# Optimization experiments

Measured on AMD Instinct MI355X. Metric: run time of the kernel, lower is better.

## Reference

```python
import jax, jax.numpy as jnp
import numpy as np

B, L, H, C, A = 8, 4096, 512, 64, 512
NEG = -1000000000.0

def setup_inputs() -> dict:
    key = jax.random.key(0)
    ks = jax.random.split(key, 6)
    hidden_states = jax.random.normal(ks[0], (B, L, H), dtype=jnp.float32)
    critical_mask = jax.random.randint(ks[1], (B, L, 1), 0, 2).astype(bool)
    count_active_channels = jax.random.randint(ks[2], (B, L, 1), 0, 64).astype(jnp.int32)
    channel_activity = jax.random.normal(ks[3], (B, L, C), dtype=jnp.float32)
    proj_w = jax.random.normal(ks[4], (H, A), dtype=jnp.float32) * 0.02
    proj_b = jnp.zeros((A,), dtype=jnp.float32)
    score_w = jax.random.normal(ks[5], (A, 1), dtype=jnp.float32) * 0.02
    score_b = jnp.zeros((1,), dtype=jnp.float32)
    return {"hidden_states": hidden_states, "critical_mask": critical_mask,
            "count_active_channels": count_active_channels,
            "channel_activity": channel_activity,
            "proj_w": proj_w, "proj_b": proj_b,
            "score_w": score_w, "score_b": score_b}

def reference(hidden_states, critical_mask, count_active_channels, channel_activity,
              proj_w, proj_b, score_w, score_b):
    mask = critical_mask[..., 0].astype(bool)                       # (B,L)
    count_signal = count_active_channels[..., 0].astype(hidden_states.dtype)  # (B,L)
    activity = jnp.maximum(channel_activity.astype(hidden_states.dtype), 0.0)  # (B,L,C)
    # score(tanh(proj(h)))  -> (B,L)
    logits = (jnp.tanh(hidden_states @ proj_w + proj_b) @ score_w + score_b)[..., 0]
    logits = logits + jnp.log1p(jnp.maximum(count_signal, 0.0))
    channel_mask = activity > 0                                      # (B,L,C)
    # (B,C,L) masked logits with log1p activity bias
    channel_logits = logits[:, None, :] + jnp.log1p(jnp.swapaxes(activity, 1, 2))
    channel_logits = jnp.where(jnp.swapaxes(channel_mask, 1, 2), channel_logits, NEG)
    has_channel_any = channel_mask.any(axis=1)                       # (B,C)
    weights = jax.nn.softmax(channel_logits, axis=-1)                # (B,C,L)
    weights = jnp.where(has_channel_any[..., None], weights, 0.0)
    channel_contexts = jnp.einsum('bcl,blh->bch', weights, hidden_states)  # (B,C,H)
    fallback = jnp.broadcast_to(hidden_states[:, -1:, :], channel_contexts.shape)
    channel_contexts = jnp.where(has_channel_any[..., None], channel_contexts, fallback)
    mix = activity / jnp.maximum(activity.sum(axis=2, keepdims=True), 1.0)  # (B,L,C)
    expanded_context = jnp.einsum('blc,bch->blh', mix, channel_contexts)    # (B,L,H)
    max_count = jnp.maximum(count_signal.max(axis=1, keepdims=True), 1.0)
    density_gate = 1.0 + count_signal / max_count                    # (B,L)
    attended = jnp.where(mask[..., None], expanded_context * density_gate[..., None], hidden_states)
    return attended, weights
```

## Files before the change

### kernel.cpp

```cpp
#include <hip/hip_runtime.h>
#include <hip/hip_bf16.h>
#include <math.h>

#define NEGV (-1000000000.0f)
constexpr int Bb = 8, Ll = 4096, Hh = 512, Cc = 64, Aa = 512;

typedef float f32x4 __attribute__((ext_vector_type(4)));
typedef short s16x8 __attribute__((ext_vector_type(8)));

__device__ inline ushort f2bf(float f) {
  union { float f; uint u; } v; v.f = f;
  uint u = v.u;
  return (ushort)((u + 0x7FFFu + ((u >> 16) & 1u)) >> 16);
}

__device__ __forceinline__ void gl16(const void* g, void* l) {
  __builtin_amdgcn_global_load_lds(
      reinterpret_cast<const __attribute__((address_space(1))) unsigned int*>(
          reinterpret_cast<uintptr_t>(g)),
      reinterpret_cast<__attribute__((address_space(3))) unsigned int*>(
          reinterpret_cast<uintptr_t>(l)),
      16, 0, 0);
}

__global__ __launch_bounds__(256) void k_front(
    const float* __restrict__ hid, const int* __restrict__ cnt,
    const float* __restrict__ sb, const float* __restrict__ pw,
    ushort* __restrict__ hidb, ushort* __restrict__ hidbT,
    float* __restrict__ logits, ushort* __restrict__ pwT,
    int* __restrict__ cmax) {
  __shared__ ushort sh[64 * 66];
  const int bid = blockIdx.x;
  const int tid = threadIdx.x;

  if (bid < 4096) {
    const int b = bid >> 9;
    const int rem = bid & 511;
    const int h0 = (rem >> 6) * 64;
    const int l0 = (rem & 63) * 64;
    const int lr = tid >> 6;
    const int hc = tid & 63;
#pragma unroll
    for (int i = 0; i < 16; ++i) {
      int l = lr + i * 4;
      ushort v = f2bf(hid[((size_t)(b * Ll + l0 + l)) * Hh + h0 + hc]);
      sh[l * 65 + hc] = v;
      hidb[((size_t)(b * Ll + l0 + l)) * Hh + h0 + hc] = v;
    }
    __syncthreads();
#pragma unroll
    for (int i = 0; i < 8; ++i) {
      int e = tid + i * 256;
      int ht = e >> 5, p = e & 31;
      uint v = (uint)sh[(2 * p) * 65 + ht] | ((uint)sh[(2 * p + 1) * 65 + ht] << 16);
      *(uint*)(hidbT + ((size_t)(b * Hh + h0 + ht)) * Ll + l0 + 2 * p) = v;
    }
  } else if (bid < 4160) {
    const int bx = bid - 4096;
    const int k0 = (bx >> 3) * 64, a0 = (bx & 7) * 64;
#pragma unroll
    for (int i = 0; i < 16; ++i) {
      int e = tid + i * 256;
      int kk = e >> 6, aa = e & 63;
      sh[aa * 65 + kk] = f2bf(pw[(size_t)(k0 + kk) * Aa + a0 + aa]);
    }
    __syncthreads();
#pragma unroll
    for (int i = 0; i < 16; ++i) {
      int e = tid + i * 256;
      int aa = e >> 6, kk = e & 63;
      pwT[(size_t)(a0 + aa) * Hh + k0 + kk] = sh[aa * 65 + kk];
    }
  } else if (bid < 4288) {
    int i = (bid - 4160) * 256 + tid;
    logits[i] = sb[0] + log1pf(fmaxf((float)cnt[i], 0.f));
  } else {
    int* shi = (int*)sh;
    const int b = bid - 4288;
    const int* p = cnt + b * Ll;
    int m = 0;
#pragma unroll
    for (int j = 0; j < 16; ++j) m = max(m, p[tid + j * 256]);
#pragma unroll
    for (int s = 32; s; s >>= 1) m = max(m, __shfl_xor(m, s));
    if ((tid & 63) == 0) shi[tid >> 6] = m;
    __syncthreads();
    if (tid == 0)
      cmax[b] = max(max(shi[0], shi[1]), max(shi[2], shi[3]));
  }
}

__global__ __launch_bounds__(256) void k0_gemm(
    const ushort* __restrict__ hidb, const ushort* __restrict__ pwT,
    const float* __restrict__ pb, const float* __restrict__ sw,
    float* __restrict__ logits) {
  __shared__ ushort smem[16384];
  const int bm = blockIdx.x, bn = blockIdx.y;
  const int tid = threadIdx.x;
  const int lane = tid & 63;
  const int w = tid >> 6;
  const int wm = w >> 1, wn = w & 1;
  const int lc = lane & 15, lq = lane >> 4;

  const int srow = tid >> 2;
  const int schunk = (tid & 3) * 8;
  const ushort* Ag = hidb + ((size_t)(bm * 128 + srow)) * Hh + schunk;
  const ushort* Bg = pwT + ((size_t)(bn * 128 + srow)) * Hh + schunk;
  const int wrow = 16 * w;

  f32x4 acc[4][4];
#pragma unroll
  for (int mi = 0; mi < 4; ++mi)
#pragma unroll
    for (int ni = 0; ni < 4; ++ni) acc[mi][ni] = (f32x4){0.f, 0.f, 0.f, 0.f};

  const int aoffc = (wm * 64 + lc) * 32 + lq * 8;
  const int boffc = (wn * 64 + lc) * 32 + lq * 8;

#define K0_STAGE(buf, kb)                                   \
  do {                                                      \
    const ushort* ag = Ag + (kb) * 32;                      \
    const ushort* bg = Bg + (kb) * 32;                      \
    ushort* la = smem + (buf) * 4096 + wrow * 32;           \
    ushort* lb = smem + 8192 + (buf) * 4096 + wrow * 32;    \
    gl16(ag, la);                                           \
    gl16(ag + 64 * Hh, la + 64 * 32);                       \
    gl16(bg, lb);                                           \
    gl16(bg + 64 * Hh, lb + 64 * 32);                       \
  } while (0)

  K0_STAGE(0, 0);
  __syncthreads();

  int buf = 0;
  for (int kb = 0; kb < 16; ++kb) {
    if (kb < 15) K0_STAGE(buf ^ 1, kb + 1);
    const ushort* Ab = smem + buf * 4096;
    const ushort* Bt = smem + 8192 + buf * 4096;
    s16x8 af[4], bfr[4];
#pragma unroll
    for (int mi = 0; mi < 4; ++mi)
      af[mi] = *(const s16x8*)(Ab + aoffc + mi * 512);
#pragma unroll
    for (int ni = 0; ni < 4; ++ni)
      bfr[ni] = *(const s16x8*)(Bt + boffc + ni * 512);
#pragma unroll
    for (int mi = 0; mi < 4; ++mi)
#pragma unroll
      for (int ni = 0; ni < 4; ++ni)
        acc[mi][ni] = __builtin_amdgcn_mfma_f32_16x16x32_bf16(
            af[mi], bfr[ni], acc[mi][ni], 0, 0, 0);
    __syncthreads();
    buf ^= 1;
  }
#undef K0_STAGE

  float pbv[4], swv[4];
#pragma unroll
  for (int ni = 0; ni < 4; ++ni) {
    int n = bn * 128 + wn * 64 + ni * 16 + lc;
    pbv[ni] = pb[n];
    swv[ni] = sw[n];
  }
#pragma unroll
  for (int mi = 0; mi < 4; ++mi) {
#pragma unroll
    for (int r = 0; r < 4; ++r) {
      float s = 0.f;
#pragma unroll
      for (int ni = 0; ni < 4; ++ni) {
        float x = acc[mi][ni][r] + pbv[ni];
        float e = __expf(2.f * x);
        float th = 1.f - 2.f / (e + 1.f);
        s = fmaf(th, swv[ni], s);
      }
      s += __shfl_xor(s, 1);
      s += __shfl_xor(s, 2);
      s += __shfl_xor(s, 4);
      s += __shfl_xor(s, 8);
      if (lc == 0) {
        int m = bm * 128 + wm * 64 + mi * 16 + lq * 4 + r;
        atomicAdd(&logits[m], s);
      }
    }
  }
}

__global__ void k2_transpose(const float* __restrict__ act,
                             float* __restrict__ actT,
                             float* __restrict__ dinv) {
  __shared__ float t64[64][65];
  const int b = blockIdx.x >> 6;
  const int l0 = (blockIdx.x & 63) * 64;
  const int tid = threadIdx.x;
#pragma unroll
  for (int i = 0; i < 16; ++i) {
    int e = tid + i * 256;
    int l = e >> 6, c = e & 63;
    float v = act[((size_t)(b * Ll + l0 + l)) * Cc + c];
    t64[l][c] = fmaxf(v, 0.f);
  }
  __syncthreads();
  if (tid < 64) {
    float s = 0.f;
#pragma unroll 8
    for (int c = 0; c < 64; ++c) s += t64[tid][c];
    dinv[b * Ll + l0 + tid] = 1.0f / fmaxf(s, 1.0f);
  }
#pragma unroll
  for (int i = 0; i < 16; ++i) {
    int e = tid + i * 256;
    int c = e >> 6, lq = e & 63;
    actT[((size_t)(b * Cc + c)) * Ll + l0 + lq] = t64[lq][c];
  }
}

__global__ void k3_softmax(const float* __restrict__ actT,
                           const float* __restrict__ logits,
                           float* __restrict__ wout,
                           ushort* __restrict__ wb16,
                           int* __restrict__ hasany) {
  __shared__ float rmax[4], rcnt[4], rsum[4];
  const int bid = blockIdx.x;
  const int b = bid >> 6;
  const int tid = threadIdx.x;
  const float* arow = actT + (size_t)bid * Ll;

  float xs[16];
  float lmax = NEGV, fcnt = 0.f;
#pragma unroll
  for (int i = 0; i < 16; ++i) {
    int l = tid + i * 256;
    float a = arow[l];
    float x;
    if (a > 0.f) {
      x = logits[b * Ll + l] + log1pf(a);
      fcnt += 1.f;
    } else {
      x = NEGV;
    }
    xs[i] = x;
    lmax = fmaxf(lmax, x);
  }
#pragma unroll
  for (int m = 32; m >= 1; m >>= 1) {
    lmax = fmaxf(lmax, __shfl_xor(lmax, m));
    fcnt += __shfl_xor(fcnt, m);
  }
  if ((tid & 63) == 0) { rmax[tid >> 6] = lmax; rcnt[tid >> 6] = fcnt; }
  __syncthreads();
  float m4 = fmaxf(fmaxf(rmax[0], rmax[1]), fmaxf(rmax[2], rmax[3]));
  float call = rcnt[0] + rcnt[1] + rcnt[2] + rcnt[3];

  float lsum = 0.f;
#pragma unroll
  for (int i = 0; i < 16; ++i) {
    float e = expf(xs[i] - m4);
    xs[i] = e;
    lsum += e;
  }
#pragma unroll
  for (int m = 32; m >= 1; m >>= 1) lsum += __shfl_xor(lsum, m);
  if ((tid & 63) == 0) rsum[tid >> 6] = lsum;
  __syncthreads();
  float s = rsum[0] + rsum[1] + rsum[2] + rsum[3];
  int any = call > 0.5f;
  float inv = any ? 1.0f / s : 0.f;
#pragma unroll
  for (int i = 0; i < 16; ++i) {
    float wv = xs[i] * inv;
    wout[(size_t)bid * Ll + tid + i * 256] = wv;
    wb16[(size_t)bid * Ll + tid + i * 256] = f2bf(wv);
  }
  if (tid == 0) hasany[bid] = any;
}

__global__ __launch_bounds__(256) void k5_mfma(
    const ushort* __restrict__ wb16, const ushort* __restrict__ hidbT,
    float* __restrict__ pbuf) {
  const int b = blockIdx.x, nt = blockIdx.y, kz = blockIdx.z;
  const int tid = threadIdx.x;
  const int w = tid >> 6, lane = tid & 63;
  const int lc = lane & 15, lq = lane >> 4;
  const int h0 = nt * 128 + w * 32;

  f32x4 acc[4][2];
#pragma unroll
  for (int mi = 0; mi < 4; ++mi)
#pragma unroll
    for (int ni = 0; ni < 2; ++ni) acc[mi][ni] = (f32x4){0.f, 0.f, 0.f, 0.f};

  const ushort* Abase =
      wb16 + (size_t)b * Cc * Ll + (size_t)lc * Ll + kz * 256 + lq * 8;
  const ushort* Bbase =
      hidbT + ((size_t)(b * Hh + h0 + lc)) * Ll + kz * 256 + lq * 8;

#pragma unroll 2
  for (int kb = 0; kb < 8; ++kb) {
    s16x8 af[4];
#pragma unroll
    for (int mi = 0; mi < 4; ++mi)
      af[mi] = *(const s16x8*)(Abase + (size_t)mi * 16 * Ll + kb * 32);
    s16x8 bfv[2];
#pragma unroll
    for (int ni = 0; ni < 2; ++ni)
      bfv[ni] = *(const s16x8*)(Bbase + (size_t)ni * 16 * Ll + kb * 32);
#pragma unroll
    for (int mi = 0; mi < 4; ++mi)
#pragma unroll
      for (int ni = 0; ni < 2; ++ni)
        acc[mi][ni] = __builtin_amdgcn_mfma_f32_16x16x32_bf16(
            af[mi], bfv[ni], acc[mi][ni], 0, 0, 0);
  }

  const size_t obase = ((size_t)(kz * Bb + b)) * Cc * Hh;
#pragma unroll
  for (int mi = 0; mi < 4; ++mi)
#pragma unroll
    for (int ni = 0; ni < 2; ++ni)
#pragma unroll
      for (int r = 0; r < 4; ++r)
        pbuf[obase + (size_t)(mi * 16 + lq * 4 + r) * Hh + h0 + ni * 16 + lc] =
            acc[mi][ni][r];
}

__global__ void k6_reduce(const float* __restrict__ pbuf,
                          const int* __restrict__ hasany,
                          const float* __restrict__ hid,
                          float* __restrict__ cctx) {
  int idx = blockIdx.x * 256 + threadIdx.x;
  float s = 0.f;
#pragma unroll
  for (int z = 0; z < 16; ++z) s += pbuf[(size_t)z * 262144 + idx];
  int bc = idx >> 9, b = idx >> 15, h = idx & 511;
  cctx[idx] = hasany[bc] ? s : hid[((size_t)(b * Ll + Ll - 1)) * Hh + h];
}

__global__ __launch_bounds__(256) void k7_out(
    const float* __restrict__ hid, const float* __restrict__ act,
    const float* __restrict__ dinv, const float* __restrict__ cctx,
    const int* __restrict__ mask, const int* __restrict__ cnt,
    const int* __restrict__ cmax, float* __restrict__ out) {
  __shared__ float cct[64][128];
  __shared__ float mixs[64][64];
  __shared__ float gateb[64];
  __shared__ int maskb[64];
  const int b = blockIdx.x;
  const int l0 = blockIdx.y * 64;
  const int h0 = blockIdx.z * 128;
  const int tid = threadIdx.x;
  const int w = tid >> 6;

  {
    const float* g = cctx + (size_t)(b * Cc + (tid >> 5)) * Hh + h0 + (tid & 31) * 4;
    float* lb = &cct[0][0] + (2 * w) * 128;
#pragma unroll
    for (int i = 0; i < 8; ++i)
      gl16(g + (size_t)(i * 8) * Hh, lb + i * 8 * 128);
  }
#pragma unroll
  for (int i = 0; i < 4; ++i) {
    int e = tid + i * 256;
    int t = e >> 4, c4 = (e & 15) * 4;
    float4 a4 = *(const float4*)(act + ((size_t)(b * Ll + l0 + t)) * Cc + c4);
    float dv = dinv[b * Ll + l0 + t];
    a4.x = fmaxf(a4.x, 0.f) * dv;
    a4.y = fmaxf(a4.y, 0.f) * dv;
    a4.z = fmaxf(a4.z, 0.f) * dv;
    a4.w = fmaxf(a4.w, 0.f) * dv;
    *(float4*)&mixs[t][c4] = a4;
  }
  if (tid < 64) {
    int l = l0 + tid;
    maskb[tid] = mask[b * Ll + l];
    gateb[tid] = 1.0f + (float)cnt[b * Ll + l] / fmaxf((float)cmax[b], 1.0f);
  }
  __syncthreads();

  const int hcol = (tid & 31) * 4;
  const int tok0 = (tid >> 5) * 8;

  f32x4 acc[8];
#pragma unroll
  for (int t = 0; t < 8; ++t) acc[t] = (f32x4){0.f, 0.f, 0.f, 0.f};

#pragma unroll 4
  for (int c0 = 0; c0 < 64; c0 += 4) {
    f32x4 cv0 = *(const f32x4*)&cct[c0 + 0][hcol];
    f32x4 cv1 = *(const f32x4*)&cct[c0 + 1][hcol];
    f32x4 cv2 = *(const f32x4*)&cct[c0 + 2][hcol];
    f32x4 cv3 = *(const f32x4*)&cct[c0 + 3][hcol];
#pragma unroll
    for (int t = 0; t < 8; ++t) {
      f32x4 mv = *(const f32x4*)&mixs[tok0 + t][c0];
      f32x4 a = acc[t];
      a = cv0 * mv.x + a;
      a = cv1 * mv.y + a;
      a = cv2 * mv.z + a;
      a = cv3 * mv.w + a;
      acc[t] = a;
    }
  }

#pragma unroll
  for (int t = 0; t < 8; ++t) {
    int tok = tok0 + t;
    size_t off = ((size_t)(b * Ll + l0 + tok)) * Hh + h0 + hcol;
    f32x4 o;
    if (maskb[tok]) {
      o = acc[t] * gateb[tok];
    } else {
      o = *(const f32x4*)(hid + off);
    }
    *(f32x4*)(out + off) = o;
  }
}

extern "C" void kernel_launch(void* const* d_in, const int* in_sizes, int n_in,
                              void* d_out, int out_size, void* d_ws,
                              size_t ws_size, hipStream_t stream) {
  const float* hid = (const float*)d_in[0];
  const int* mask = (const int*)d_in[1];
  const int* cnt = (const int*)d_in[2];
  const float* act = (const float*)d_in[3];
  const float* pw = (const float*)d_in[4];
  const float* pb = (const float*)d_in[5];
  const float* sw = (const float*)d_in[6];
  const float* sb = (const float*)d_in[7];

  float* out_att = (float*)d_out;
  float* out_w = out_att + (size_t)Bb * Ll * Hh;

  float* ws = (float*)d_ws;
  float* cctx = ws;
  int* cmaxi = (int*)(ws + 262144);
  float* logits = ws + 262152;
  float* actT = ws + 294920;
  float* dinv = ws + 2392072;
  int* hasany = (int*)(ws + 2424840);
  ushort* pwT = (ushort*)(ws + 2425352);
  ushort* wb16 = (ushort*)(ws + 2556424);
  float* pbuf = ws + 3605000;

  ushort* hidb = (ushort*)out_att;
  ushort* hidbT = (ushort*)(out_att + 8388608);

  k_front<<<4296, 256, 0, stream>>>(hid, cnt, sb, pw, hidb, hidbT, logits,
                                    pwT, cmaxi);
  k0_gemm<<<dim3(256, 4), 256, 0, stream>>>(hidb, pwT, pb, sw, logits);
  k2_transpose<<<512, 256, 0, stream>>>(act, actT, dinv);
  k3_softmax<<<512, 256, 0, stream>>>(actT, logits, out_w, wb16, hasany);
  k5_mfma<<<dim3(8, 4, 16), 256, 0, stream>>>(wb16, hidbT, pbuf);
  k6_reduce<<<1024, 256, 0, stream>>>(pbuf, hasany, hid, cctx);
  k7_out<<<dim3(8, 64, 4), 256, 0, stream>>>(hid, act, dinv, cctx, mask, cnt,
                                             cmaxi, out_att);
}
```

Before: 257.5 us.

## Double split-K in channel GEMM, prefetch its operands, vectorize front transpose

The channel-context MFMA kernel now splits the L reduction into 32 slices instead of 16, doubling the grid and giving each block half the K work. The loop is unrolled by hand so the next step's fragments load while the current MFMAs run, and the reduce kernel sums 32 partial buffers. The front bf16 conversion/transpose block now reads float2 and writes packed uint and uint4 stores, with LDS padding changed to 66. The extra split-K slices double the partial-buffer traffic and workspace use, which could offset the gain in occupancy.

Measured after the change: 260.0 us. About the same (+1.0%).

```diff
diff --git a/kernel.cpp b/kernel.cpp
--- a/kernel.cpp
+++ b/kernel.cpp
@@ -38,23 +38,31 @@
     const int rem = bid & 511;
     const int h0 = (rem >> 6) * 64;
     const int l0 = (rem & 63) * 64;
-    const int lr = tid >> 6;
-    const int hc = tid & 63;
-#pragma unroll
-    for (int i = 0; i < 16; ++i) {
-      int l = lr + i * 4;
-      ushort v = f2bf(hid[((size_t)(b * Ll + l0 + l)) * Hh + h0 + hc]);
-      sh[l * 65 + hc] = v;
-      hidb[((size_t)(b * Ll + l0 + l)) * Hh + h0 + hc] = v;
+    const int lr = tid >> 5;
+    const int hc2 = (tid & 31) * 2;
+#pragma unroll
+    for (int i = 0; i < 8; ++i) {
+      int l = lr * 8 + i;
+      float2 f =
+          *(const float2*)(hid + ((size_t)(b * Ll + l0 + l)) * Hh + h0 + hc2);
+      ushort v0 = f2bf(f.x), v1 = f2bf(f.y);
+      *(uint*)(hidb + ((size_t)(b * Ll + l0 + l)) * Hh + h0 + hc2) =
+          (uint)v0 | ((uint)v1 << 16);
+      sh[l * 66 + hc2] = v0;
+      sh[l * 66 + hc2 + 1] = v1;
     }
     __syncthreads();
-#pragma unroll
-    for (int i = 0; i < 8; ++i) {
-      int e = tid + i * 256;
-      int ht = e >> 5, p = e & 31;
-      uint v = (uint)sh[(2 * p) * 65 + ht] | ((uint)sh[(2 * p + 1) * 65 + ht] << 16);
-      *(uint*)(hidbT + ((size_t)(b * Hh + h0 + ht)) * Ll + l0 + 2 * p) = v;
-    }
+    const int ht = tid >> 2;
+    const int d0 = (tid & 3) * 8;
+    uint v[8];
+#pragma unroll
+    for (int k = 0; k < 8; ++k) {
+      int p = d0 + k;
+      v[k] = (uint)sh[(2 * p) * 66 + ht] | ((uint)sh[(2 * p + 1) * 66 + ht] << 16);
+    }
+    ushort* dst = hidbT + ((size_t)(b * Hh + h0 + ht)) * Ll + l0 + 2 * d0;
+    *(uint4*)dst = (uint4){v[0], v[1], v[2], v[3]};
+    *(uint4*)(dst + 8) = (uint4){v[4], v[5], v[6], v[7]};
   } else if (bid < 4160) {
     const int bx = bid - 4096;
     const int k0 = (bx >> 3) * 64, a0 = (bx & 7) * 64;
@@ -85,8 +93,7 @@
     for (int s = 32; s; s >>= 1) m = max(m, __shfl_xor(m, s));
     if ((tid & 63) == 0) shi[tid >> 6] = m;
     __syncthreads();
-    if (tid == 0)
-      cmax[b] = max(max(shi[0], shi[1]), max(shi[2], shi[3]));
+    if (tid == 0) cmax[b] = max(max(shi[0], shi[1]), max(shi[2], shi[3]));
   }
 }
 
@@ -291,27 +298,37 @@
     for (int ni = 0; ni < 2; ++ni) acc[mi][ni] = (f32x4){0.f, 0.f, 0.f, 0.f};
 
   const ushort* Abase =
-      wb16 + (size_t)b * Cc * Ll + (size_t)lc * Ll + kz * 256 + lq * 8;
+      wb16 + (size_t)b * Cc * Ll + (size_t)lc * Ll + kz * 128 + lq * 8;
   const ushort* Bbase =
-      hidbT + ((size_t)(b * Hh + h0 + lc)) * Ll + kz * 256 + lq * 8;
-
-#pragma unroll 2
-  for (int kb = 0; kb < 8; ++kb) {
-    s16x8 af[4];
-#pragma unroll
-    for (int mi = 0; mi < 4; ++mi)
-      af[mi] = *(const s16x8*)(Abase + (size_t)mi * 16 * Ll + kb * 32);
-    s16x8 bfv[2];
-#pragma unroll
-    for (int ni = 0; ni < 2; ++ni)
-      bfv[ni] = *(const s16x8*)(Bbase + (size_t)ni * 16 * Ll + kb * 32);
-#pragma unroll
-    for (int mi = 0; mi < 4; ++mi)
-#pragma unroll
-      for (int ni = 0; ni < 2; ++ni)
-        acc[mi][ni] = __builtin_amdgcn_mfma_f32_16x16x32_bf16(
-            af[mi], bfv[ni], acc[mi][ni], 0, 0, 0);
-  }
+      hidbT + ((size_t)(b * Hh + h0 + lc)) * Ll + kz * 128 + lq * 8;
+
+#define K5_LOAD(kb, A, Bv)                                                 \
+  do {                                                                     \
+    _Pragma("unroll") for (int mi = 0; mi < 4; ++mi) A[mi] =               \
+        *(const s16x8*)(Abase + (size_t)mi * 16 * Ll + (kb) * 32);         \
+    _Pragma("unroll") for (int ni = 0; ni < 2; ++ni) Bv[ni] =              \
+        *(const s16x8*)(Bbase + (size_t)ni * 16 * Ll + (kb) * 32);         \
+  } while (0)
+
+#define K5_MFMA(A, Bv)                                                     \
+  do {                                                                     \
+    _Pragma("unroll") for (int mi = 0; mi < 4; ++mi)                       \
+        _Pragma("unroll") for (int ni = 0; ni < 2; ++ni) acc[mi][ni] =     \
+            __builtin_amdgcn_mfma_f32_16x16x32_bf16(A[mi], Bv[ni],         \
+                                                    acc[mi][ni], 0, 0, 0); \
+  } while (0)
+
+  s16x8 aF[4], bF[2], aG[4], bG[2];
+  K5_LOAD(0, aF, bF);
+  K5_LOAD(1, aG, bG);
+  K5_MFMA(aF, bF);
+  K5_LOAD(2, aF, bF);
+  K5_MFMA(aG, bG);
+  K5_LOAD(3, aG, bG);
+  K5_MFMA(aF, bF);
+  K5_MFMA(aG, bG);
+#undef K5_LOAD
+#undef K5_MFMA
 
   const size_t obase = ((size_t)(kz * Bb + b)) * Cc * Hh;
 #pragma unroll
@@ -331,7 +348,7 @@
   int idx = blockIdx.x * 256 + threadIdx.x;
   float s = 0.f;
 #pragma unroll
-  for (int z = 0; z < 16; ++z) s += pbuf[(size_t)z * 262144 + idx];
+  for (int z = 0; z < 32; ++z) s += pbuf[(size_t)z * 262144 + idx];
   int bc = idx >> 9, b = idx >> 15, h = idx & 511;
   cctx[idx] = hasany[bc] ? s : hid[((size_t)(b * Ll + Ll - 1)) * Hh + h];
 }
@@ -450,7 +467,7 @@
   k0_gemm<<<dim3(256, 4), 256, 0, stream>>>(hidb, pwT, pb, sw, logits);
   k2_transpose<<<512, 256, 0, stream>>>(act, actT, dinv);
   k3_softmax<<<512, 256, 0, stream>>>(actT, logits, out_w, wb16, hasany);
-  k5_mfma<<<dim3(8, 4, 16), 256, 0, stream>>>(wb16, hidbT, pbuf);
+  k5_mfma<<<dim3(8, 4, 32), 256, 0, stream>>>(wb16, hidbT, pbuf);
   k6_reduce<<<1024, 256, 0, stream>>>(pbuf, hasany, hid, cctx);
   k7_out<<<dim3(8, 64, 4), 256, 0, stream>>>(hid, act, dinv, cctx, mask, cnt,
                                              cmaxi, out_att);
```
